# Performance work log

Measured on AMD Instinct MI355X. Metric: run time of the kernel, lower is better.

Reference implementation:

```python
import jax, jax.numpy as jnp
import numpy as np

K = 3
PAD = 1


def conv3x3(x, w, b):
    # x: [B,Ci,H,W], w: [Co,Ci,3,3] -> [B,Co,H,W]
    y = jax.lax.conv_general_dilated(
        x, w, window_strides=(1, 1), padding=((PAD, PAD), (PAD, PAD)),
        dimension_numbers=('NCHW', 'OIHW', 'NCHW'))
    return y + b[None, :, None, None]


def _gather(x_flat, idx):
    # x_flat: [C, H*W], idx: [K2*H*W] -> [C, K2*H*W]
    return x_flat[:, idx]


def deform_sample(x, off_x, off_y, mask):
    """Modulated deformable im2col (DCNv2, dg=1, stride=1, pad=1, dil=1).
    x: [B,C,H,W]; off_x, off_y, mask: [B,K2,H,W] -> cols [B,C,K2,H,W]."""
    B, C, H, W = x.shape
    K2 = K * K
    # static kernel-tap displacements relative to output pixel
    dy = jnp.repeat(jnp.arange(K), K) - PAD          # [K2]
    dx = jnp.tile(jnp.arange(K), K) - PAD            # [K2]
    gy = jnp.arange(H)[:, None].astype(x.dtype)      # [H,1]
    gx = jnp.arange(W)[None, :].astype(x.dtype)      # [1,W]
    ys = gy[None, None] + dy[None, :, None, None].astype(x.dtype) + off_y  # [B,K2,H,W]
    xs = gx[None, None] + dx[None, :, None, None].astype(x.dtype) + off_x
    y0 = jnp.floor(ys)
    x0 = jnp.floor(xs)
    wy1 = ys - y0
    wx1 = xs - x0
    xf = x.reshape(B, C, H * W)
    val = jnp.zeros((B, C, K2, H, W), x.dtype)
    for oy, ox in ((0, 0), (0, 1), (1, 0), (1, 1)):
        yy = y0 + oy
        xx = x0 + ox
        wgt = (wy1 if oy else 1.0 - wy1) * (wx1 if ox else 1.0 - wx1)
        valid = ((yy >= 0) & (yy < H) & (xx >= 0) & (xx < W)).astype(x.dtype)
        idx = (jnp.clip(yy, 0, H - 1) * W + jnp.clip(xx, 0, W - 1)).astype(jnp.int32)
        g = jax.vmap(_gather)(xf, idx.reshape(B, -1)).reshape(B, C, K2, H, W)
        val = val + (wgt * valid)[:, None] * g
    return val * mask[:, None]  # modulation, broadcast over C


def reference(x, feat, w_off, b_off, w_def, b_def):
    # offset/mask prediction conv (3*K2 channels), chunked as in the torch module
    om = conv3x3(feat, w_off, b_off)
    off_x, off_y, m = jnp.split(om, 3, axis=1)   # each [B,K2,H,W]
    mask = jax.nn.sigmoid(m)
    cols = deform_sample(x, off_x, off_y, mask)  # [B,C,K2,H,W]
    O = w_def.shape[0]
    out = jnp.einsum('bckhw,ock->bohw', cols, w_def.reshape(O, -1, K * K))
    out = out + b_def[None, :, None, None]
    return jax.nn.relu(out)


def setup_inputs() -> dict:
    key = jax.random.key(0)
    k1, k2, k3, k4 = jax.random.split(key, 4)
    B, C, O, H, W = 4, 64, 64, 128, 128
    K2 = K * K
    x = jax.random.normal(k1, (B, C, H, W), jnp.float32)
    feat = jax.random.normal(k2, (B, C, H, W), jnp.float32)
    # offset conv params: small init so offsets stay near zero (as in practice)
    w_off = jax.random.normal(k3, (3 * K2, C, 3, 3), jnp.float32) * 0.01
    b_off = jnp.zeros((3 * K2,), jnp.float32)
    w_def = jax.random.normal(k4, (O, C, 3, 3), jnp.float32) * (1.0 / np.sqrt(C * K2))
    b_def = jnp.zeros((O,), jnp.float32)
    return {"x": x, "feat": feat, "w_off": w_off, "b_off": b_off,
            "w_def": w_def, "b_def": b_def}
```

## Files before the change

### kernel.cpp

```cpp
#include <hip/hip_runtime.h>
#include <math.h>

#define Bn 4
#define Cn 64
#define On 64
#define Hn 128
#define Wn 128
#define HWn (Hn * Wn)

typedef __attribute__((ext_vector_type(8))) short s16x8;
typedef __attribute__((ext_vector_type(4))) float f32x4;

__device__ __forceinline__ unsigned short f2bf(float f) {
    unsigned u = __float_as_uint(f);
    u += 0x7fffu + ((u >> 16) & 1u);
    return (unsigned short)(u >> 16);
}
__device__ __forceinline__ float bf2f(unsigned short u) {
    return __uint_as_float(((unsigned)u) << 16);
}

__global__ __launch_bounds__(256) void transpose_all(const float* __restrict__ x,
                                                     const float* __restrict__ feat,
                                                     const float* __restrict__ wdef,
                                                     const float* __restrict__ woff,
                                                     ushort* __restrict__ xt,
                                                     ushort* __restrict__ ft,
                                                     ushort* __restrict__ wdT2,
                                                     ushort* __restrict__ woT2) {
    int t = threadIdx.x;
    if (blockIdx.z == 2) {
        int id = (blockIdx.y * gridDim.x + blockIdx.x) * 256 + t;
        if (id < 36864) {
            int c2 = id & 31, oc = (id >> 5) & 63, ks = id >> 11;
            int k = ks % 9, s = ks / 9;
            wdT2[id] = f2bf(wdef[(oc * 64 + s * 32 + c2) * 9 + k]);
        } else if (id < 55296) {
            int i2 = id - 36864;
            int c2 = i2 & 31, oc = (i2 >> 5) & 31, ks = i2 >> 10;
            int k = ks % 9, s = ks / 9;
            woT2[i2] = (oc < 27) ? f2bf(woff[(oc * 64 + s * 32 + c2) * 9 + k]) : (ushort)0;
        }
        return;
    }
    __shared__ float tile[64][65];
    const float* src = blockIdx.z ? feat : x;
    ushort* dst0 = blockIdx.z ? ft : xt;
    int b = blockIdx.y, hw0 = blockIdx.x * 64;
    int lane = t & 63, grp = t >> 6;
    const float* xb = src + (size_t)b * Cn * HWn;
#pragma unroll
    for (int i = 0; i < 16; ++i) {
        int c = grp * 16 + i;
        tile[lane][c] = xb[(size_t)c * HWn + hw0 + lane];
    }
    __syncthreads();
#pragma unroll
    for (int jj = 0; jj < 2; ++jj) {
        int px = jj * 32 + (t >> 3), ch = t & 7;
        s16x8 p;
#pragma unroll
        for (int j = 0; j < 8; ++j) p[j] = (short)f2bf(tile[px][ch * 8 + j]);
        *(s16x8*)(dst0 + ((size_t)(b * HWn + hw0 + px)) * Cn + ch * 8) = p;
    }
}

__global__ __launch_bounds__(256, 3) void mega_kernel(const ushort* __restrict__ xt,
                                                      const ushort* __restrict__ ft,
                                                      const ushort* __restrict__ wdT2,
                                                      const ushort* __restrict__ woT2,
                                                      const float* __restrict__ b_off,
                                                      const float* __restrict__ b_def,
                                                      float* __restrict__ out) {
    __shared__ __align__(16) char smem[47104];
    ushort* s_win = (ushort*)smem;
    ushort* s_ft = (ushort*)(smem + 28672);
    float* s_om = (float*)(smem + 28672);
    float* s_out = (float*)(smem + 28672);

    int t = threadIdx.x;
    int wv = t >> 6, l = t & 63;
    int q = l >> 4, r = l & 15;
    int blk = (blockIdx.x & 7) * 128 + (blockIdx.x >> 3);
    int b = blk >> 8;
    int gi = blk & 255;
    int h = (gi >> 2) << 1;
    int wbase = (gi & 3) << 5;
    int rowoff = wv >> 1, pxh = wv & 1;
    int hrow = h + rowoff;
    int pxi = pxh * 16 + r;
    float pxif = (float)pxi;
    float rowofff = (float)rowoff;
    const ushort* xt_b = xt + (size_t)b * HWn * Cn;
    const ushort* ft_b = ft + (size_t)b * HWn * Cn;

#pragma unroll
    for (int i = 0; i < 5; ++i) {
        int jb = i * 256 + wv * 64;
        if (jb < 1152) {
            int j = jb + l;
            int lin = j >> 3, slot = j & 7;
            int cidx = (slot - lin) & 7;
            int row = lin / 36, col = lin - row * 36;
            int rs = min(max(h - 1 + row, 0), Hn - 1);
            int cs = min(max(wbase - 2 + col, 0), Wn - 1);
            const ushort* gp = ft_b + (size_t)(rs * Wn + cs) * Cn + cidx * 8;
            __builtin_amdgcn_global_load_lds(
                (const __attribute__((address_space(1))) unsigned int*)gp,
                (__attribute__((address_space(3))) unsigned int*)(s_ft + (size_t)jb * 8),
                16, 0, 0);
        }
    }
#pragma unroll
    for (int i = 0; i < 7; ++i) {
        int jb = i * 256 + wv * 64;
        int j = jb + l;
        int lin = j >> 3, slot = j & 7;
        int linc = min(lin, 215);
        int cidx = (slot - lin) & 7;
        int row = linc / 36, col = linc - row * 36;
        int rs = min(max(h - 2 + row, 0), Hn - 1);
        int cs = min(max(wbase - 2 + col, 0), Wn - 1);
        const ushort* gp = xt_b + (size_t)(rs * Wn + cs) * Cn + cidx * 8;
        __builtin_amdgcn_global_load_lds(
            (const __attribute__((address_space(1))) unsigned int*)gp,
            (__attribute__((address_space(3))) unsigned int*)(s_win + (size_t)jb * 8),
            16, 0, 0);
    }
    asm volatile("s_waitcnt vmcnt(7)" ::: "memory");
    __builtin_amdgcn_s_barrier();

    f32x4 zero = {0.f, 0.f, 0.f, 0.f};
    s16x8 zz = {0, 0, 0, 0, 0, 0, 0, 0};

    f32x4 acc2[2];
    acc2[0] = zero; acc2[1] = zero;
    {
        int pxg = wv * 16 + r;
        int rg = pxg >> 5, cg = pxg & 31;
#pragma unroll 3
        for (int k = 0; k < 9; ++k) {
            int dy = k / 3 - 1, dx = k % 3 - 1;
            int y = h + rg + dy;
            bool yv = (y >= 0) && (y < Hn);
            int xx = wbase + cg + dx;
            bool valid = yv && (xx >= 0) && (xx < Wn);
            int lin = (rg + dy + 1) * 36 + cg + dx + 2;
#pragma unroll
            for (int s = 0; s < 2; ++s) {
                int c = s * 4 + q;
                s16x8 av = *(const s16x8*)&s_ft[lin * 64 + (((c + lin) & 7) << 3)];
                av = valid ? av : zz;
#pragma unroll
                for (int ot = 0; ot < 2; ++ot) {
                    s16x8 bv = *(const s16x8*)(woT2 + (size_t)s * 9216
                                               + (size_t)(k * 32 + ot * 16 + r) * 32 + q * 8);
                    acc2[ot] = __builtin_amdgcn_mfma_f32_16x16x32_bf16(av, bv, acc2[ot], 0, 0, 0);
                }
            }
        }
    }
    __syncthreads();

#pragma unroll
    for (int ot = 0; ot < 2; ++ot) {
        int oc = ot * 16 + r;
        if (oc < 27) {
            float bo = b_off[oc];
#pragma unroll
            for (int reg = 0; reg < 4; ++reg) {
                int p = wv * 16 + q * 4 + reg;
                float v = acc2[ot][reg] + bo;
                if (oc >= 18) v = 1.f / (1.f + __expf(-v));
                s_om[oc * 64 + p] = v;
            }
        }
    }
    __syncthreads();

    float omv[27];
#pragma unroll
    for (int o = 0; o < 27; ++o) omv[o] = s_om[o * 64 + rowoff * 32 + pxi];
    bool okp = true;
#pragma unroll
    for (int k = 0; k < 9; ++k) {
        float uy = (float)(k / 3 - 1) + omv[9 + k];
        float ux = pxif + (float)(k % 3 - 1) + omv[k];
        okp = okp && (uy >= -2.f - rowofff) && (uy < 3.f - rowofff)
                  && (ux >= -2.f) && (ux < 33.f);
    }
    int fast = __all(okp) ? 1 : 0;

    f32x4 acc[4];
    acc[0] = zero; acc[1] = zero; acc[2] = zero; acc[3] = zero;

    if (fast) {
#pragma unroll 3
        for (int k = 0; k < 9; ++k) {
            float uy = (float)(k / 3 - 1) + omv[9 + k];
            float ux = pxif + (float)(k % 3 - 1) + omv[k];
            float mv = omv[18 + k];
            float y0f = floorf(uy), x0f = floorf(ux);
            float fy = uy - y0f, fx = ux - x0f;
            int iy = (int)y0f + 2 + rowoff;
            int ix = (int)x0f + 2;
            int yab = hrow + (int)y0f, xab = wbase + (int)x0f;
            bool vy0 = (yab >= 0) && (yab < Hn);
            bool vy1 = (yab + 1 >= 0) && (yab + 1 < Hn);
            bool vx0 = (xab >= 0) && (xab < Wn);
            bool vx1 = (xab + 1 >= 0) && (xab + 1 < Wn);
            float g0 = (vy0 && vx0) ? (1.f - fy) * (1.f - fx) * mv : 0.f;
            float g1 = (vy0 && vx1) ? (1.f - fy) * fx * mv : 0.f;
            float g2 = (vy1 && vx0) ? fy * (1.f - fx) * mv : 0.f;
            float g3 = (vy1 && vx1) ? fy * fx * mv : 0.f;
            int l0 = iy * 36 + ix, l1 = l0 + 1, l2 = l0 + 36, l3 = l0 + 37;
            s16x8 bw[2][4];
#pragma unroll
            for (int s = 0; s < 2; ++s)
#pragma unroll
                for (int ot = 0; ot < 4; ++ot)
                    bw[s][ot] = *(const s16x8*)(wdT2 + (size_t)s * 18432
                                                + (size_t)(k * 64 + ot * 16 + r) * 32 + q * 8);
            s16x8 af[2];
#pragma unroll
            for (int s = 0; s < 2; ++s) {
                int c = s * 4 + q;
                s16x8 q0 = *(const s16x8*)&s_win[l0 * 64 + (((c + l0) & 7) << 3)];
                s16x8 q1 = *(const s16x8*)&s_win[l1 * 64 + (((c + l1) & 7) << 3)];
                s16x8 q2 = *(const s16x8*)&s_win[l2 * 64 + (((c + l2) & 7) << 3)];
                s16x8 q3 = *(const s16x8*)&s_win[l3 * 64 + (((c + l3) & 7) << 3)];
                s16x8 p;
#pragma unroll
                for (int j = 0; j < 8; ++j) {
                    float rr = g0 * bf2f((unsigned short)q0[j]) + g1 * bf2f((unsigned short)q1[j])
                             + g2 * bf2f((unsigned short)q2[j]) + g3 * bf2f((unsigned short)q3[j]);
                    p[j] = (short)f2bf(rr);
                }
                af[s] = p;
            }
#pragma unroll
            for (int s = 0; s < 2; ++s)
#pragma unroll
                for (int ot = 0; ot < 4; ++ot)
                    acc[ot] = __builtin_amdgcn_mfma_f32_16x16x32_bf16(af[s], bw[s][ot], acc[ot], 0, 0, 0);
        }
    } else {
#pragma unroll 1
        for (int k = 0; k < 9; ++k) {
            float ys = (float)(hrow + k / 3 - 1) + omv[9 + k];
            float xs = (float)(wbase + pxi + k % 3 - 1) + omv[k];
            float mv = omv[18 + k];
            float y0f = floorf(ys), x0f = floorf(xs);
            float fy = ys - y0f, fx = xs - x0f;
            int y0 = (int)y0f, x0 = (int)x0f;
            float g[4];
            int a[4];
#pragma unroll
            for (int n = 0; n < 4; ++n) {
                int yy = y0 + (n >> 1), xx = x0 + (n & 1);
                bool valid = (yy >= 0) && (yy < Hn) && (xx >= 0) && (xx < Wn);
                float wgt = ((n >> 1) ? fy : 1.f - fy) * ((n & 1) ? fx : 1.f - fx) * mv;
                g[n] = valid ? wgt : 0.f;
                int yc = min(max(yy, 0), Hn - 1), xc = min(max(xx, 0), Wn - 1);
                a[n] = (yc * Wn + xc) * Cn;
            }
#pragma unroll
            for (int s = 0; s < 2; ++s) {
                int c = s * 32 + q * 8;
                s16x8 q0 = *(const s16x8*)(xt_b + a[0] + c);
                s16x8 q1 = *(const s16x8*)(xt_b + a[1] + c);
                s16x8 q2 = *(const s16x8*)(xt_b + a[2] + c);
                s16x8 q3 = *(const s16x8*)(xt_b + a[3] + c);
                s16x8 af;
#pragma unroll
                for (int j = 0; j < 8; ++j) {
                    float rr = g[0] * bf2f((unsigned short)q0[j]) + g[1] * bf2f((unsigned short)q1[j])
                             + g[2] * bf2f((unsigned short)q2[j]) + g[3] * bf2f((unsigned short)q3[j]);
                    af[j] = (short)f2bf(rr);
                }
#pragma unroll
                for (int ot = 0; ot < 4; ++ot) {
                    s16x8 bv = *(const s16x8*)(wdT2 + (size_t)s * 18432
                                               + (size_t)(k * 64 + ot * 16 + r) * 32 + q * 8);
                    acc[ot] = __builtin_amdgcn_mfma_f32_16x16x32_bf16(af, bv, acc[ot], 0, 0, 0);
                }
            }
        }
    }
    __syncthreads();

#pragma unroll
    for (int ot = 0; ot < 4; ++ot) {
        int oc = ot * 16 + r;
        float bv = b_def[oc];
        f32x4 vv;
#pragma unroll
        for (int reg = 0; reg < 4; ++reg) vv[reg] = fmaxf(acc[ot][reg] + bv, 0.f);
        *(f32x4*)&s_out[oc * 68 + rowoff * 32 + pxh * 16 + q * 4] = vv;
    }
    __syncthreads();
    {
        int px = t & 63, og = t >> 6;
        int rg = h + (px >> 5);
        float* ob = out + ((size_t)b * On) * HWn + rg * Wn + wbase + (px & 31);
#pragma unroll
        for (int j = 0; j < 16; ++j) {
            int oc = og * 16 + j;
            ob[(size_t)oc * HWn] = s_out[oc * 68 + px];
        }
    }
}

extern "C" void kernel_launch(void* const* d_in, const int* in_sizes, int n_in,
                              void* d_out, int out_size, void* d_ws, size_t ws_size,
                              hipStream_t stream) {
    const float* x = (const float*)d_in[0];
    const float* feat = (const float*)d_in[1];
    const float* w_off = (const float*)d_in[2];
    const float* b_off = (const float*)d_in[3];
    const float* w_def = (const float*)d_in[4];
    const float* b_def = (const float*)d_in[5];
    float* out = (float*)d_out;

    char* ws = (char*)d_ws;
    ushort* xt = (ushort*)ws;
    ushort* ft = (ushort*)(ws + 8388608);
    ushort* wdT2 = (ushort*)(ws + 16777216);
    ushort* woT2 = (ushort*)(ws + 16850944);

    hipLaunchKernelGGL(transpose_all, dim3(HWn / 64, Bn, 3), dim3(256), 0, stream,
                       x, feat, w_def, w_off, xt, ft, wdT2, woT2);
    hipLaunchKernelGGL(mega_kernel, dim3((Bn * HWn) / 64), dim3(256), 0, stream,
                       xt, ft, wdT2, woT2, b_off, b_def, out);
}
```

Before: 123.0 us.

## Drop LDS window staging and read conv and deform taps directly from global

Removes the async global-to-LDS staging of the feature and input windows. The offset conv and the deformable bilinear gather now read bf16 NHWC data straight from global memory, relying on the L1 and L2 caches, and the LDS-backed fast path with its __all check is deleted. Shared memory drops from about 46KB to 17KB, which may raise occupancy. The cost is more global and cache traffic per tap, and the loss of the LDS reuse and the overlap of loads with compute.

```diff
diff --git a/kernel.cpp b/kernel.cpp
--- a/kernel.cpp
+++ b/kernel.cpp
@@ -72,11 +72,9 @@
                                                       const float* __restrict__ b_off,
                                                       const float* __restrict__ b_def,
                                                       float* __restrict__ out) {
-    __shared__ __align__(16) char smem[47104];
-    ushort* s_win = (ushort*)smem;
-    ushort* s_ft = (ushort*)(smem + 28672);
-    float* s_om = (float*)(smem + 28672);
-    float* s_out = (float*)(smem + 28672);
+    __shared__ __align__(16) char smem[17408];
+    float* s_om = (float*)smem;
+    float* s_out = (float*)smem;
 
     int t = threadIdx.x;
     int wv = t >> 6, l = t & 63;
@@ -89,46 +87,8 @@
     int rowoff = wv >> 1, pxh = wv & 1;
     int hrow = h + rowoff;
     int pxi = pxh * 16 + r;
-    float pxif = (float)pxi;
-    float rowofff = (float)rowoff;
     const ushort* xt_b = xt + (size_t)b * HWn * Cn;
     const ushort* ft_b = ft + (size_t)b * HWn * Cn;
-
-#pragma unroll
-    for (int i = 0; i < 5; ++i) {
-        int jb = i * 256 + wv * 64;
-        if (jb < 1152) {
-            int j = jb + l;
-            int lin = j >> 3, slot = j & 7;
-            int cidx = (slot - lin) & 7;
-            int row = lin / 36, col = lin - row * 36;
-            int rs = min(max(h - 1 + row, 0), Hn - 1);
-            int cs = min(max(wbase - 2 + col, 0), Wn - 1);
-            const ushort* gp = ft_b + (size_t)(rs * Wn + cs) * Cn + cidx * 8;
-            __builtin_amdgcn_global_load_lds(
-                (const __attribute__((address_space(1))) unsigned int*)gp,
-                (__attribute__((address_space(3))) unsigned int*)(s_ft + (size_t)jb * 8),
-                16, 0, 0);
-        }
-    }
-#pragma unroll
-    for (int i = 0; i < 7; ++i) {
-        int jb = i * 256 + wv * 64;
-        int j = jb + l;
-        int lin = j >> 3, slot = j & 7;
-        int linc = min(lin, 215);
-        int cidx = (slot - lin) & 7;
-        int row = linc / 36, col = linc - row * 36;
-        int rs = min(max(h - 2 + row, 0), Hn - 1);
-        int cs = min(max(wbase - 2 + col, 0), Wn - 1);
-        const ushort* gp = xt_b + (size_t)(rs * Wn + cs) * Cn + cidx * 8;
-        __builtin_amdgcn_global_load_lds(
-            (const __attribute__((address_space(1))) unsigned int*)gp,
-            (__attribute__((address_space(3))) unsigned int*)(s_win + (size_t)jb * 8),
-            16, 0, 0);
-    }
-    asm volatile("s_waitcnt vmcnt(7)" ::: "memory");
-    __builtin_amdgcn_s_barrier();
 
     f32x4 zero = {0.f, 0.f, 0.f, 0.f};
     s16x8 zz = {0, 0, 0, 0, 0, 0, 0, 0};
@@ -145,11 +105,12 @@
             bool yv = (y >= 0) && (y < Hn);
             int xx = wbase + cg + dx;
             bool valid = yv && (xx >= 0) && (xx < Wn);
-            int lin = (rg + dy + 1) * 36 + cg + dx + 2;
+            int ys_ = min(max(y, 0), Hn - 1);
+            int xs_ = min(max(xx, 0), Wn - 1);
+            const ushort* ap = ft_b + (size_t)(ys_ * Wn + xs_) * Cn;
 #pragma unroll
             for (int s = 0; s < 2; ++s) {
-                int c = s * 4 + q;
-                s16x8 av = *(const s16x8*)&s_ft[lin * 64 + (((c + lin) & 7) << 3)];
+                s16x8 av = *(const s16x8*)(ap + (s * 4 + q) * 8);
                 av = valid ? av : zz;
 #pragma unroll
                 for (int ot = 0; ot < 2; ++ot) {
@@ -160,7 +121,6 @@
             }
         }
     }
-    __syncthreads();
 
 #pragma unroll
     for (int ot = 0; ot < 2; ++ot) {
@@ -180,110 +140,49 @@
 
     float omv[27];
 #pragma unroll
-    for (int o = 0; o < 27; ++o) omv[o] = s_om[o * 64 + rowoff * 32 + pxi];
-    bool okp = true;
-#pragma unroll
-    for (int k = 0; k < 9; ++k) {
-        float uy = (float)(k / 3 - 1) + omv[9 + k];
-        float ux = pxif + (float)(k % 3 - 1) + omv[k];
-        okp = okp && (uy >= -2.f - rowofff) && (uy < 3.f - rowofff)
-                  && (ux >= -2.f) && (ux < 33.f);
-    }
-    int fast = __all(okp) ? 1 : 0;
+    for (int o = 0; o < 27; ++o) omv[o] = s_om[o * 64 + wv * 16 + r];
+    __syncthreads();
 
     f32x4 acc[4];
     acc[0] = zero; acc[1] = zero; acc[2] = zero; acc[3] = zero;
-
-    if (fast) {
-#pragma unroll 3
-        for (int k = 0; k < 9; ++k) {
-            float uy = (float)(k / 3 - 1) + omv[9 + k];
-            float ux = pxif + (float)(k % 3 - 1) + omv[k];
-            float mv = omv[18 + k];
-            float y0f = floorf(uy), x0f = floorf(ux);
-            float fy = uy - y0f, fx = ux - x0f;
-            int iy = (int)y0f + 2 + rowoff;
-            int ix = (int)x0f + 2;
-            int yab = hrow + (int)y0f, xab = wbase + (int)x0f;
-            bool vy0 = (yab >= 0) && (yab < Hn);
-            bool vy1 = (yab + 1 >= 0) && (yab + 1 < Hn);
-            bool vx0 = (xab >= 0) && (xab < Wn);
-            bool vx1 = (xab + 1 >= 0) && (xab + 1 < Wn);
-            float g0 = (vy0 && vx0) ? (1.f - fy) * (1.f - fx) * mv : 0.f;
-            float g1 = (vy0 && vx1) ? (1.f - fy) * fx * mv : 0.f;
-            float g2 = (vy1 && vx0) ? fy * (1.f - fx) * mv : 0.f;
-            float g3 = (vy1 && vx1) ? fy * fx * mv : 0.f;
-            int l0 = iy * 36 + ix, l1 = l0 + 1, l2 = l0 + 36, l3 = l0 + 37;
-            s16x8 bw[2][4];
-#pragma unroll
-            for (int s = 0; s < 2; ++s)
-#pragma unroll
-                for (int ot = 0; ot < 4; ++ot)
-                    bw[s][ot] = *(const s16x8*)(wdT2 + (size_t)s * 18432
-                                                + (size_t)(k * 64 + ot * 16 + r) * 32 + q * 8);
-            s16x8 af[2];
-#pragma unroll
-            for (int s = 0; s < 2; ++s) {
-                int c = s * 4 + q;
-                s16x8 q0 = *(const s16x8*)&s_win[l0 * 64 + (((c + l0) & 7) << 3)];
-                s16x8 q1 = *(const s16x8*)&s_win[l1 * 64 + (((c + l1) & 7) << 3)];
-                s16x8 q2 = *(const s16x8*)&s_win[l2 * 64 + (((c + l2) & 7) << 3)];
-                s16x8 q3 = *(const s16x8*)&s_win[l3 * 64 + (((c + l3) & 7) << 3)];
-                s16x8 p;
-#pragma unroll
-                for (int j = 0; j < 8; ++j) {
-                    float rr = g0 * bf2f((unsigned short)q0[j]) + g1 * bf2f((unsigned short)q1[j])
-                             + g2 * bf2f((unsigned short)q2[j]) + g3 * bf2f((unsigned short)q3[j]);
-                    p[j] = (short)f2bf(rr);
-                }
-                af[s] = p;
-            }
-#pragma unroll
-            for (int s = 0; s < 2; ++s)
-#pragma unroll
-                for (int ot = 0; ot < 4; ++ot)
-                    acc[ot] = __builtin_amdgcn_mfma_f32_16x16x32_bf16(af[s], bw[s][ot], acc[ot], 0, 0, 0);
-        }
-    } else {
 #pragma unroll 1
-        for (int k = 0; k < 9; ++k) {
-            float ys = (float)(hrow + k / 3 - 1) + omv[9 + k];
-            float xs = (float)(wbase + pxi + k % 3 - 1) + omv[k];
-            float mv = omv[18 + k];
-            float y0f = floorf(ys), x0f = floorf(xs);
-            float fy = ys - y0f, fx = xs - x0f;
-            int y0 = (int)y0f, x0 = (int)x0f;
-            float g[4];
-            int a[4];
-#pragma unroll
-            for (int n = 0; n < 4; ++n) {
-                int yy = y0 + (n >> 1), xx = x0 + (n & 1);
-                bool valid = (yy >= 0) && (yy < Hn) && (xx >= 0) && (xx < Wn);
-                float wgt = ((n >> 1) ? fy : 1.f - fy) * ((n & 1) ? fx : 1.f - fx) * mv;
-                g[n] = valid ? wgt : 0.f;
-                int yc = min(max(yy, 0), Hn - 1), xc = min(max(xx, 0), Wn - 1);
-                a[n] = (yc * Wn + xc) * Cn;
-            }
-#pragma unroll
-            for (int s = 0; s < 2; ++s) {
-                int c = s * 32 + q * 8;
-                s16x8 q0 = *(const s16x8*)(xt_b + a[0] + c);
-                s16x8 q1 = *(const s16x8*)(xt_b + a[1] + c);
-                s16x8 q2 = *(const s16x8*)(xt_b + a[2] + c);
-                s16x8 q3 = *(const s16x8*)(xt_b + a[3] + c);
-                s16x8 af;
-#pragma unroll
-                for (int j = 0; j < 8; ++j) {
-                    float rr = g[0] * bf2f((unsigned short)q0[j]) + g[1] * bf2f((unsigned short)q1[j])
-                             + g[2] * bf2f((unsigned short)q2[j]) + g[3] * bf2f((unsigned short)q3[j]);
-                    af[j] = (short)f2bf(rr);
-                }
-#pragma unroll
-                for (int ot = 0; ot < 4; ++ot) {
-                    s16x8 bv = *(const s16x8*)(wdT2 + (size_t)s * 18432
-                                               + (size_t)(k * 64 + ot * 16 + r) * 32 + q * 8);
-                    acc[ot] = __builtin_amdgcn_mfma_f32_16x16x32_bf16(af, bv, acc[ot], 0, 0, 0);
-                }
+    for (int k = 0; k < 9; ++k) {
+        float ys = (float)(hrow + k / 3 - 1) + omv[9 + k];
+        float xs = (float)(wbase + pxi + k % 3 - 1) + omv[k];
+        float mv = omv[18 + k];
+        float y0f = floorf(ys), x0f = floorf(xs);
+        float fy = ys - y0f, fx = xs - x0f;
+        int y0 = (int)y0f, x0 = (int)x0f;
+        float g[4];
+        int a[4];
+#pragma unroll
+        for (int n = 0; n < 4; ++n) {
+            int yy = y0 + (n >> 1), xx = x0 + (n & 1);
+            bool valid = (yy >= 0) && (yy < Hn) && (xx >= 0) && (xx < Wn);
+            float wgt = ((n >> 1) ? fy : 1.f - fy) * ((n & 1) ? fx : 1.f - fx) * mv;
+            g[n] = valid ? wgt : 0.f;
+            int yc = min(max(yy, 0), Hn - 1), xc = min(max(xx, 0), Wn - 1);
+            a[n] = (yc * Wn + xc) * Cn;
+        }
+#pragma unroll
+        for (int s = 0; s < 2; ++s) {
+            int c = s * 32 + q * 8;
+            s16x8 q0 = *(const s16x8*)(xt_b + a[0] + c);
+            s16x8 q1 = *(const s16x8*)(xt_b + a[1] + c);
+            s16x8 q2 = *(const s16x8*)(xt_b + a[2] + c);
+            s16x8 q3 = *(const s16x8*)(xt_b + a[3] + c);
+            s16x8 af;
+#pragma unroll
+            for (int j = 0; j < 8; ++j) {
+                float rr = g[0] * bf2f((unsigned short)q0[j]) + g[1] * bf2f((unsigned short)q1[j])
+                         + g[2] * bf2f((unsigned short)q2[j]) + g[3] * bf2f((unsigned short)q3[j]);
+                af[j] = (short)f2bf(rr);
+            }
+#pragma unroll
+            for (int ot = 0; ot < 4; ++ot) {
+                s16x8 bv = *(const s16x8*)(wdT2 + (size_t)s * 18432
+                                           + (size_t)(k * 64 + ot * 16 + r) * 32 + q * 8);
+                acc[ot] = __builtin_amdgcn_mfma_f32_16x16x32_bf16(af, bv, acc[ot], 0, 0, 0);
             }
         }
     }
```

Measured after the change: 168.1 us. 36.7% more time.

## Read offset-conv inputs from global memory, shrink LDS, use packed bf16 converts

Applied to the files above, without the earlier changes.

The offset-prediction conv no longer stages the feat window in LDS. Each lane reads its 16-byte feat slice straight from global or cache, which removes a barrier and cuts LDS from 47KB to 35.5KB so more blocks can be resident per CU. The output staging buffer now aliases the start of LDS. Separately, the bilinear-sampled values are packed to bf16 with the hardware v_cvt_pk_bf16_f32 instruction instead of manual round-to-nearest bit arithmetic. The trade-off is more uncoalesced global reads for the conv taps and a possible shift in the hazards of reusing the s_win/s_out region.

```diff
diff --git a/kernel.cpp b/kernel.cpp
--- a/kernel.cpp
+++ b/kernel.cpp
@@ -10,6 +10,7 @@
 
 typedef __attribute__((ext_vector_type(8))) short s16x8;
 typedef __attribute__((ext_vector_type(4))) float f32x4;
+typedef __attribute__((ext_vector_type(4))) unsigned int u32x4;
 
 __device__ __forceinline__ unsigned short f2bf(float f) {
     unsigned u = __float_as_uint(f);
@@ -18,6 +19,16 @@
 }
 __device__ __forceinline__ float bf2f(unsigned short u) {
     return __uint_as_float(((unsigned)u) << 16);
+}
+__device__ __forceinline__ s16x8 pack8(const float* rr) {
+    u32x4 pk;
+#pragma unroll
+    for (int jj = 0; jj < 4; ++jj) {
+        unsigned w;
+        asm("v_cvt_pk_bf16_f32 %0, %1, %2" : "=v"(w) : "v"(rr[2 * jj]), "v"(rr[2 * jj + 1]));
+        pk[jj] = w;
+    }
+    return __builtin_bit_cast(s16x8, pk);
 }
 
 __global__ __launch_bounds__(256) void transpose_all(const float* __restrict__ x,
@@ -72,11 +83,10 @@
                                                       const float* __restrict__ b_off,
                                                       const float* __restrict__ b_def,
                                                       float* __restrict__ out) {
-    __shared__ __align__(16) char smem[47104];
+    __shared__ __align__(16) char smem[35584];
     ushort* s_win = (ushort*)smem;
-    ushort* s_ft = (ushort*)(smem + 28672);
     float* s_om = (float*)(smem + 28672);
-    float* s_out = (float*)(smem + 28672);
+    float* s_out = (float*)smem;
 
     int t = threadIdx.x;
     int wv = t >> 6, l = t & 63;
@@ -95,23 +105,6 @@
     const ushort* ft_b = ft + (size_t)b * HWn * Cn;
 
 #pragma unroll
-    for (int i = 0; i < 5; ++i) {
-        int jb = i * 256 + wv * 64;
-        if (jb < 1152) {
-            int j = jb + l;
-            int lin = j >> 3, slot = j & 7;
-            int cidx = (slot - lin) & 7;
-            int row = lin / 36, col = lin - row * 36;
-            int rs = min(max(h - 1 + row, 0), Hn - 1);
-            int cs = min(max(wbase - 2 + col, 0), Wn - 1);
-            const ushort* gp = ft_b + (size_t)(rs * Wn + cs) * Cn + cidx * 8;
-            __builtin_amdgcn_global_load_lds(
-                (const __attribute__((address_space(1))) unsigned int*)gp,
-                (__attribute__((address_space(3))) unsigned int*)(s_ft + (size_t)jb * 8),
-                16, 0, 0);
-        }
-    }
-#pragma unroll
     for (int i = 0; i < 7; ++i) {
         int jb = i * 256 + wv * 64;
         int j = jb + l;
@@ -127,8 +120,6 @@
             (__attribute__((address_space(3))) unsigned int*)(s_win + (size_t)jb * 8),
             16, 0, 0);
     }
-    asm volatile("s_waitcnt vmcnt(7)" ::: "memory");
-    __builtin_amdgcn_s_barrier();
 
     f32x4 zero = {0.f, 0.f, 0.f, 0.f};
     s16x8 zz = {0, 0, 0, 0, 0, 0, 0, 0};
@@ -145,11 +136,12 @@
             bool yv = (y >= 0) && (y < Hn);
             int xx = wbase + cg + dx;
             bool valid = yv && (xx >= 0) && (xx < Wn);
-            int lin = (rg + dy + 1) * 36 + cg + dx + 2;
+            int ys_ = min(max(y, 0), Hn - 1);
+            int xs_ = min(max(xx, 0), Wn - 1);
+            const ushort* ap = ft_b + (size_t)(ys_ * Wn + xs_) * Cn;
 #pragma unroll
             for (int s = 0; s < 2; ++s) {
-                int c = s * 4 + q;
-                s16x8 av = *(const s16x8*)&s_ft[lin * 64 + (((c + lin) & 7) << 3)];
+                s16x8 av = *(const s16x8*)(ap + (s * 4 + q) * 8);
                 av = valid ? av : zz;
 #pragma unroll
                 for (int ot = 0; ot < 2; ++ot) {
@@ -160,7 +152,6 @@
             }
         }
     }
-    __syncthreads();
 
 #pragma unroll
     for (int ot = 0; ot < 2; ++ot) {
@@ -229,14 +220,13 @@
                 s16x8 q1 = *(const s16x8*)&s_win[l1 * 64 + (((c + l1) & 7) << 3)];
                 s16x8 q2 = *(const s16x8*)&s_win[l2 * 64 + (((c + l2) & 7) << 3)];
                 s16x8 q3 = *(const s16x8*)&s_win[l3 * 64 + (((c + l3) & 7) << 3)];
-                s16x8 p;
+                float rr[8];
 #pragma unroll
                 for (int j = 0; j < 8; ++j) {
-                    float rr = g0 * bf2f((unsigned short)q0[j]) + g1 * bf2f((unsigned short)q1[j])
-                             + g2 * bf2f((unsigned short)q2[j]) + g3 * bf2f((unsigned short)q3[j]);
-                    p[j] = (short)f2bf(rr);
+                    rr[j] = g0 * bf2f((unsigned short)q0[j]) + g1 * bf2f((unsigned short)q1[j])
+                          + g2 * bf2f((unsigned short)q2[j]) + g3 * bf2f((unsigned short)q3[j]);
                 }
-                af[s] = p;
+                af[s] = pack8(rr);
             }
 #pragma unroll
             for (int s = 0; s < 2; ++s)
@@ -271,13 +261,13 @@
                 s16x8 q1 = *(const s16x8*)(xt_b + a[1] + c);
                 s16x8 q2 = *(const s16x8*)(xt_b + a[2] + c);
                 s16x8 q3 = *(const s16x8*)(xt_b + a[3] + c);
-                s16x8 af;
+                float rr[8];
 #pragma unroll
                 for (int j = 0; j < 8; ++j) {
-                    float rr = g[0] * bf2f((unsigned short)q0[j]) + g[1] * bf2f((unsigned short)q1[j])
-                             + g[2] * bf2f((unsigned short)q2[j]) + g[3] * bf2f((unsigned short)q3[j]);
-                    af[j] = (short)f2bf(rr);
+                    rr[j] = g[0] * bf2f((unsigned short)q0[j]) + g[1] * bf2f((unsigned short)q1[j])
+                          + g[2] * bf2f((unsigned short)q2[j]) + g[3] * bf2f((unsigned short)q3[j]);
                 }
+                s16x8 af = pack8(rr);
 #pragma unroll
                 for (int ot = 0; ot < 4; ++ot) {
                     s16x8 bv = *(const s16x8*)(wdT2 + (size_t)s * 18432
```

Result: slower. 135.0 us (+9.8%).
